# Kernel optimization log

Hardware: AMD Instinct MI355X
Metric: run time of the kernel (lower is better)

The kernel has to match this reference:

```python
import jax, jax.numpy as jnp
import numpy as np

B = 32            # graphs in batch
NPG = 2048        # nodes per graph (equal-size graphs -> static topk sizes)
N = B * NPG
DEG = 8
E = N * DEG
IN = 64
H1 = 2 * IN       # 128
H2 = 2 * H1       # 256
K1 = NPG // 2     # SAGPooling ratio=0.5
K2 = K1 // 2
EPS = 1e-5


def _lin(k, fi, fo):
    s = 1.0 / np.sqrt(fi)
    return jax.random.uniform(k, (fi, fo), jnp.float32, -s, s)


def setup_inputs() -> dict:
    key = jax.random.key(0)
    ks = jax.random.split(key, 24)
    x = jax.random.normal(ks[0], (N, IN), jnp.float32)
    # edges strictly within each graph
    eg = jnp.repeat(jnp.arange(B, dtype=jnp.int32), NPG * DEG)
    src = eg * NPG + jax.random.randint(ks[1], (E,), 0, NPG, jnp.int32)
    tgt = eg * NPG + jax.random.randint(ks[2], (E,), 0, NPG, jnp.int32)
    edge_index = jnp.stack([src, tgt])
    batch = jnp.repeat(jnp.arange(B, dtype=jnp.int32), NPG)
    return {
        "x": x, "edge_index": edge_index, "batch": batch,
        # SAGEConv1: lin_l (neighbors, with bias) + lin_r (root, no bias)
        "W1l": _lin(ks[3], IN, H1), "b1l": jnp.zeros((H1,), jnp.float32),
        "W1r": _lin(ks[4], IN, H1),
        "bn1_g": jnp.ones((H1,), jnp.float32), "bn1_b": jnp.zeros((H1,), jnp.float32),
        # SAGPooling1 scorer = GraphConv(H1, 1): lin_rel (sum-agg, bias) + lin_root
        "p1_Wrel": _lin(ks[5], H1, 1), "p1_brel": jnp.zeros((1,), jnp.float32),
        "p1_Wroot": _lin(ks[6], H1, 1),
        "W2l": _lin(ks[7], H1, H2), "b2l": jnp.zeros((H2,), jnp.float32),
        "W2r": _lin(ks[8], H1, H2),
        "bn2_g": jnp.ones((H2,), jnp.float32), "bn2_b": jnp.zeros((H2,), jnp.float32),
        "p2_Wrel": _lin(ks[9], H2, 1), "p2_brel": jnp.zeros((1,), jnp.float32),
        "p2_Wroot": _lin(ks[10], H2, 1),
        "Wlin": _lin(ks[11], H2, 2), "blin": jnp.zeros((2,), jnp.float32),
    }


def sage_conv(x, src, tgt, emask, Wl, bl, Wr, n):
    # PyG SAGEConv: mean-aggregate x_j over valid incoming edges, then lin_l(agg)+lin_r(x)
    msg = x[src] * emask[:, None]
    s = jax.ops.segment_sum(msg, tgt, num_segments=n)
    cnt = jax.ops.segment_sum(emask, tgt, num_segments=n)
    mean = s / jnp.maximum(cnt, 1.0)[:, None]
    return mean @ Wl + bl + x @ Wr


def graph_conv_score(x, src, tgt, emask, Wrel, brel, Wroot, n):
    # PyG GraphConv (sum aggregation), out_channels=1
    s = jax.ops.segment_sum(x[src] * emask[:, None], tgt, num_segments=n)
    return (s @ Wrel + brel + x @ Wroot)[:, 0]


def batch_norm(x, g, b):
    m = x.mean(0)
    v = jnp.mean((x - m) ** 2, 0)  # biased var, as BatchNorm1d training
    return (x - m) * jax.lax.rsqrt(v + EPS) * g + b


def sag_pool(x, src, tgt, emask, score, npg, k):
    # per-graph top-k by score; x_kept scaled by tanh(score); edges re-filtered via mask
    vals, idx = jax.lax.top_k(score.reshape(B, npg), k)          # [B,k]
    perm = (jnp.arange(B, dtype=jnp.int32)[:, None] * npg + idx.astype(jnp.int32)).reshape(-1)
    xnew = x[perm] * jnp.tanh(vals.reshape(-1))[:, None]
    mapping = jnp.full((x.shape[0],), -1, jnp.int32).at[perm].set(
        jnp.arange(B * k, dtype=jnp.int32))
    ns, nt = mapping[src], mapping[tgt]
    valid = emask * ((ns >= 0) & (nt >= 0)).astype(emask.dtype)
    return xnew, jnp.maximum(ns, 0), jnp.maximum(nt, 0), valid


def reference(x, edge_index, batch, W1l, b1l, W1r, bn1_g, bn1_b,
              p1_Wrel, p1_brel, p1_Wroot, W2l, b2l, W2r, bn2_g, bn2_b,
              p2_Wrel, p2_brel, p2_Wroot, Wlin, blin):
    src, tgt = edge_index[0], edge_index[1]
    emask = jnp.ones((src.shape[0],), x.dtype)

    h = sage_conv(x, src, tgt, emask, W1l, b1l, W1r, N)
    h = jax.nn.relu(batch_norm(h, bn1_g, bn1_b))
    s1 = graph_conv_score(h, src, tgt, emask, p1_Wrel, p1_brel, p1_Wroot, N)
    h, src, tgt, emask = sag_pool(h, src, tgt, emask, s1, NPG, K1)

    n1 = B * K1
    h = sage_conv(h, src, tgt, emask, W2l, b2l, W2r, n1)
    h = jax.nn.relu(batch_norm(h, bn2_g, bn2_b))
    s2 = graph_conv_score(h, src, tgt, emask, p2_Wrel, p2_brel, p2_Wroot, n1)
    h, src, tgt, emask = sag_pool(h, src, tgt, emask, s2, K1, K2)

    batch2 = jnp.repeat(jnp.arange(B, dtype=jnp.int32), K2)
    pooled = jax.ops.segment_sum(h, batch2, num_segments=B) / jnp.asarray(K2, h.dtype)
    out = jax.nn.relu(pooled) @ Wlin + blin
    return jax.nn.softmax(out, axis=1)
```

## Files before the change

kernel.cpp:

```cpp
#include <hip/hip_runtime.h>
#include <math.h>

#define Bg   32
#define NPGc 2048
#define Nn   (Bg*NPGc)
#define DEGc 8
#define Ee   (Nn*DEGc)
#define INc  64
#define H1c  128
#define H2c  256
#define K1c  1024
#define K2c  512
#define N1c  (Bg*K1c)
#define N2c  (Bg*K2c)
#define SLAB 64

typedef __attribute__((ext_vector_type(8))) short short8;
typedef __attribute__((ext_vector_type(4))) float f32x4;

__device__ __forceinline__ ushort f2bf(float f) {
    uint u = __float_as_uint(f);
    uint r = (u + 0x7fffu + ((u >> 16) & 1u)) >> 16;
    return (ushort)r;
}
__device__ __forceinline__ float bf2f(ushort v) { return __uint_as_float((uint)v << 16); }
__device__ __forceinline__ float bfhi(uint v) { return __uint_as_float(v & 0xffff0000u); }
__device__ __forceinline__ float bflo(uint v) { return __uint_as_float(v << 16); }
__device__ __forceinline__ uint fkey(float f) {
    uint u = __float_as_uint(f);
    return u ^ ((uint)((int)u >> 31) | 0x80000000u);
}

__global__ void init_kernel(int4* __restrict__ wc1, int4* __restrict__ wc2,
                            int4* __restrict__ dstats) {
    int id = blockIdx.x * blockDim.x + threadIdx.x;
    int4 z = {0, 0, 0, 0};
    if (id < 16384) { wc1[id] = z; return; }
    id -= 16384;
    if (id < 8192)  { wc2[id] = z; return; }
    id -= 8192;
    if (id < 384)   { dstats[id] = z; }
}

__global__ void prep2_kernel(const float* __restrict__ x,
                             const int* __restrict__ src, const int* __restrict__ tgt,
                             const float* __restrict__ W1l, const float* __restrict__ W1r,
                             const float* __restrict__ W2l, const float* __restrict__ W2r,
                             ushort* __restrict__ T1l, ushort* __restrict__ T1r,
                             ushort* __restrict__ T2l, ushort* __restrict__ T2r,
                             ushort* __restrict__ xb, int* __restrict__ wc1,
                             int* __restrict__ col1) {
    int id = blockIdx.x * blockDim.x + threadIdx.x;
    if (id < Ee) {
        int t = tgt[id];
        int p = atomicAdd(&wc1[t], 1);
        col1[t * SLAB + p] = src[id];
        return;
    }
    id -= Ee;
    if (id < 8192) {
        int c = id / 64, k = id % 64;
        T1l[id] = f2bf(W1l[k * 128 + c]);
        T1r[id] = f2bf(W1r[k * 128 + c]);
        return;
    }
    id -= 8192;
    if (id < 32768) {
        int c = id / 128, k = id % 128;
        T2l[id] = f2bf(W2l[k * 256 + c]);
        T2r[id] = f2bf(W2r[k * 256 + c]);
        return;
    }
    id -= 32768;
    if (id < Nn * 16) {
        float4 v = ((const float4*)x)[id];
        ushort4 o; o.x = f2bf(v.x); o.y = f2bf(v.y); o.z = f2bf(v.z); o.w = f2bf(v.w);
        ((ushort4*)xb)[id] = o;
    }
}
#define PREP2_TOTAL (Ee + 8192 + 32768 + Nn*16)

__device__ __forceinline__ void acc8(float* a, uint4 v) {
    a[0] += bflo(v.x); a[1] += bfhi(v.x);
    a[2] += bflo(v.y); a[3] += bfhi(v.y);
    a[4] += bflo(v.z); a[5] += bfhi(v.z);
    a[6] += bflo(v.w); a[7] += bfhi(v.w);
}
__device__ __forceinline__ uint4 pack8(const float* a, float inv) {
    uint4 o;
    o.x = (uint)f2bf(a[0] * inv) | ((uint)f2bf(a[1] * inv) << 16);
    o.y = (uint)f2bf(a[2] * inv) | ((uint)f2bf(a[3] * inv) << 16);
    o.z = (uint)f2bf(a[4] * inv) | ((uint)f2bf(a[5] * inv) << 16);
    o.w = (uint)f2bf(a[6] * inv) | ((uint)f2bf(a[7] * inv) << 16);
    return o;
}

__global__ void agg1_kernel(const ushort* __restrict__ xb, const int* __restrict__ deg,
                            const int* __restrict__ col, ushort* __restrict__ out) {
    int b = blockIdx.x;
    int w = ((b & 7) << 8) + (b >> 3);
    int gid = w * 256 + threadIdx.x;
    int node = gid >> 3, ln = gid & 7;
    int bg = node * SLAB, dg = deg[node];
    int4 c0 = *(const int4*)&col[bg];
    int4 c1 = *(const int4*)&col[bg + 4];
    int idx[8] = {c0.x, c0.y, c0.z, c0.w, c1.x, c1.y, c1.z, c1.w};
    float a[8] = {0.f, 0.f, 0.f, 0.f, 0.f, 0.f, 0.f, 0.f};
#pragma unroll
    for (int j = 0; j < 8; j++)
        if (j < dg) acc8(a, *(const uint4*)&xb[((size_t)idx[j] << 6) + ln * 8]);
    for (int i = bg + 8; i < bg + dg; i++)
        acc8(a, *(const uint4*)&xb[((size_t)col[i] << 6) + ln * 8]);
    int c = dg < 1 ? 1 : dg;
    *(uint4*)&out[((size_t)node << 6) + ln * 8] = pack8(a, 1.f / (float)c);
}

__global__ void agg2_kernel(const ushort* __restrict__ xb, const int* __restrict__ deg,
                            const int* __restrict__ col, ushort* __restrict__ out) {
    int b = blockIdx.x;
    int w = ((b & 7) << 8) + (b >> 3);
    int gid = w * 256 + threadIdx.x;
    int node = gid >> 4, ln = gid & 15;
    int bg = node * SLAB, dg = deg[node];
    int4 c0 = *(const int4*)&col[bg];
    int4 c1 = *(const int4*)&col[bg + 4];
    int idx[8] = {c0.x, c0.y, c0.z, c0.w, c1.x, c1.y, c1.z, c1.w};
    float a[8] = {0.f, 0.f, 0.f, 0.f, 0.f, 0.f, 0.f, 0.f};
#pragma unroll
    for (int j = 0; j < 8; j++)
        if (j < dg) acc8(a, *(const uint4*)&xb[((size_t)idx[j] << 7) + ln * 8]);
    for (int i = bg + 8; i < bg + dg; i++)
        acc8(a, *(const uint4*)&xb[((size_t)col[i] << 7) + ln * 8]);
    int c = dg < 1 ? 1 : dg;
    *(uint4*)&out[((size_t)node << 7) + ln * 8] = pack8(a, 1.f / (float)c);
}

template<int K, int COUT, int MT>
__global__ __launch_bounds__(256) void gemm_mfma_kernel(
        const ushort* __restrict__ Aagg, const ushort* __restrict__ Ax,
        const ushort* __restrict__ Wtl, const ushort* __restrict__ Wtr,
        const float* __restrict__ bias, ushort* __restrict__ out,
        double* __restrict__ dsum, double* __restrict__ dsq) {
    __shared__ ushort As[2][128][72];
    __shared__ ushort Bs[2][64][72];
    __shared__ float bsumS[2][64], bsqS[2][64];
    int bid = blockIdx.x;
    int m0 = (bid % MT) * 128;
    int c0 = (bid / MT) * 64;
    int lane = threadIdx.x & 63;
    int wid = threadIdx.x >> 6;
    int wr = (wid & 1) * 64, wc = (wid >> 1) * 32;
    int l16 = lane & 15, quad = lane >> 4;

    f32x4 acc[4][2];
#pragma unroll
    for (int a = 0; a < 4; a++)
#pragma unroll
        for (int b = 0; b < 2; b++) acc[a][b] = (f32x4){0.f, 0.f, 0.f, 0.f};

    for (int kk0 = 0; kk0 < K; kk0 += 64) {
        for (int idx = threadIdx.x; idx < 1024; idx += 256) {
            int r = idx >> 3, ck = (idx & 7) * 8;
            *(uint4*)&As[0][r][ck] = *(const uint4*)&Aagg[(size_t)(m0 + r) * K + kk0 + ck];
            *(uint4*)&As[1][r][ck] = *(const uint4*)&Ax[(size_t)(m0 + r) * K + kk0 + ck];
        }
        for (int idx = threadIdx.x; idx < 512; idx += 256) {
            int r = idx >> 3, ck = (idx & 7) * 8;
            *(uint4*)&Bs[0][r][ck] = *(const uint4*)&Wtl[(size_t)(c0 + r) * K + kk0 + ck];
            *(uint4*)&Bs[1][r][ck] = *(const uint4*)&Wtr[(size_t)(c0 + r) * K + kk0 + ck];
        }
        __syncthreads();
#pragma unroll
        for (int kk = 0; kk < 64; kk += 32) {
            short8 a[2][4], b[2][2];
#pragma unroll
            for (int s = 0; s < 2; s++)
#pragma unroll
                for (int mt = 0; mt < 4; mt++)
                    a[s][mt] = *(const short8*)&As[s][wr + mt * 16 + l16][kk + quad * 8];
#pragma unroll
            for (int s = 0; s < 2; s++)
#pragma unroll
                for (int nt = 0; nt < 2; nt++)
                    b[s][nt] = *(const short8*)&Bs[s][wc + nt * 16 + l16][kk + quad * 8];
#pragma unroll
            for (int mt = 0; mt < 4; mt++)
#pragma unroll
                for (int nt = 0; nt < 2; nt++) {
                    acc[mt][nt] = __builtin_amdgcn_mfma_f32_16x16x32_bf16(
                        a[0][mt], b[0][nt], acc[mt][nt], 0, 0, 0);
                    acc[mt][nt] = __builtin_amdgcn_mfma_f32_16x16x32_bf16(
                        a[1][mt], b[1][nt], acc[mt][nt], 0, 0, 0);
                }
        }
        __syncthreads();
    }
    float s[2] = {0.f, 0.f}, sq[2] = {0.f, 0.f};
#pragma unroll
    for (int nt = 0; nt < 2; nt++) {
        int col = c0 + wc + nt * 16 + l16;
        float bv = bias[col];
#pragma unroll
        for (int mt = 0; mt < 4; mt++)
#pragma unroll
            for (int r = 0; r < 4; r++) {
                int row = m0 + wr + mt * 16 + quad * 4 + r;
                float ov = acc[mt][nt][r] + bv;
                out[(size_t)row * COUT + col] = f2bf(ov);
                s[nt] += ov; sq[nt] += ov * ov;
            }
    }
#pragma unroll
    for (int nt = 0; nt < 2; nt++) {
        float ss = s[nt], qq = sq[nt];
        ss += __shfl_down(ss, 16); qq += __shfl_down(qq, 16);
        ss += __shfl_down(ss, 32); qq += __shfl_down(qq, 32);
        if (quad == 0) {
            bsumS[wid & 1][wc + nt * 16 + l16] = ss;
            bsqS[wid & 1][wc + nt * 16 + l16] = qq;
        }
    }
    __syncthreads();
    if (threadIdx.x < 64) {
        int c = threadIdx.x;
        atomicAdd(&dsum[c0 + c], (double)(bsumS[0][c] + bsumS[1][c]));
        atomicAdd(&dsq[c0 + c], (double)(bsqS[0][c] + bsqS[1][c]));
    }
}

template<int C>
__global__ __launch_bounds__(256) void score_kernel(const ushort* __restrict__ h,
                                                    const double* __restrict__ dsum,
                                                    const double* __restrict__ dsq,
                                                    const float* __restrict__ g,
                                                    const float* __restrict__ b,
                                                    const float* __restrict__ wrel,
                                                    const float* __restrict__ wroot,
                                                    float* __restrict__ r,
                                                    float* __restrict__ root, int n) {
    __shared__ float sc[C], sh[C], wrl[C], wrt[C];
    if ((int)threadIdx.x < C) {
        int c = threadIdx.x;
        double m = dsum[c] / (double)n;
        double var = dsq[c] / (double)n - m * m;
        float s = g[c] * (float)(1.0 / sqrt(var + 1e-5));
        sc[c] = s; sh[c] = b[c] - (float)m * s;
        wrl[c] = wrel[c]; wrt[c] = wroot[c];
    }
    __syncthreads();
    int gid = blockIdx.x * 256 + threadIdx.x;
    int node = gid >> 3, ln = gid & 7;
    float rr = 0.f, rt = 0.f;
#pragma unroll
    for (int p = 0; p < C / 64; p++) {
        int cb = p * 64 + ln * 8;
        uint4 v = *(const uint4*)&h[(size_t)node * C + cb];
        float vv[8] = {bflo(v.x), bfhi(v.x), bflo(v.y), bfhi(v.y),
                       bflo(v.z), bfhi(v.z), bflo(v.w), bfhi(v.w)};
#pragma unroll
        for (int q = 0; q < 8; q++) {
            int cc = cb + q;
            float val = fmaxf(vv[q] * sc[cc] + sh[cc], 0.f);
            rr += val * wrl[cc];
            rt += val * wrt[cc];
        }
    }
#pragma unroll
    for (int off = 4; off; off >>= 1) {
        rr += __shfl_down(rr, off);
        rt += __shfl_down(rt, off);
    }
    if (ln == 0) { r[node] = rr; root[node] = rt; }
}

__global__ void __launch_bounds__(1024) sel1_kernel(const float* __restrict__ r,
                                                    const float* __restrict__ root,
                                                    const int* __restrict__ deg,
                                                    const int* __restrict__ col,
                                                    const float* __restrict__ brel,
                                                    int* __restrict__ perm,
                                                    float* __restrict__ tval,
                                                    int* __restrict__ map) {
    __shared__ float svals[2048];
    __shared__ uint hist[257];
    __shared__ uint wsum[16];
    __shared__ uint s_b, s_rem;
    int g = blockIdx.x;
    int tid = threadIdx.x;
    int lane = tid & 63, wid = tid >> 6;
    int base = g * NPGc;
    float bv = brel[0];
#pragma unroll
    for (int j = 0; j < 2; j++) {
        int i = tid + (j << 10);
        int node = base + i;
        float acc = bv + root[node];
        int e0 = node * SLAB, dg = deg[node];
        int4 c0 = *(const int4*)&col[e0];
        int4 c1 = *(const int4*)&col[e0 + 4];
        int idx[8] = {c0.x, c0.y, c0.z, c0.w, c1.x, c1.y, c1.z, c1.w};
#pragma unroll
        for (int q = 0; q < 8; q++)
            if (q < dg) acc += r[idx[q]];
        for (int e = e0 + 8; e < e0 + dg; e++) acc += r[col[e]];
        svals[i] = acc;
    }
    if (tid < 257) hist[tid] = 0;
    __syncthreads();

    uint prefix = 0, himask = 0, rem = (uint)K1c;
    for (int shift = 24; shift >= 0; shift -= 8) {
#pragma unroll
        for (int j = 0; j < 2; j++) {
            uint kk = fkey(svals[tid + (j << 10)]);
            if ((kk & himask) == prefix) atomicAdd(&hist[(kk >> shift) & 255], 1);
        }
        __syncthreads();
        if (tid < 64) {
            int L = tid;
            uint h0 = hist[4 * L], h1 = hist[4 * L + 1], h2 = hist[4 * L + 2],
                 h3 = hist[4 * L + 3];
            uint s3 = h3, s2 = h2 + s3, s1 = h1 + s2, s0 = h0 + s1;
            uint v = s0;
            for (int off = 1; off < 64; off <<= 1) {
                uint u = __shfl_down(v, off);
                if (L + off < 64) v += u;
            }
            uint above = v - s0;
            hist[4 * L] = s0 + above;
            hist[4 * L + 1] = s1 + above;
            hist[4 * L + 2] = s2 + above;
            hist[4 * L + 3] = s3 + above;
        }
        __syncthreads();
        if (tid < 256) {
            uint sb = hist[tid], sb1 = hist[tid + 1];
            if (sb >= rem && sb1 < rem) { s_b = (uint)tid; s_rem = rem - sb1; }
        }
        __syncthreads();
        prefix |= (s_b << shift);
        rem = s_rem;
        himask |= (0xFFu << shift);
        if (tid < 256) hist[tid] = 0;
        __syncthreads();
    }
    uint thr = prefix;
    uint tieM = rem;
    uint gcnt = 0, ecnt = 0, gflags = 0, eflags = 0;
#pragma unroll
    for (int j = 0; j < 2; j++) {
        uint kk = fkey(svals[tid + (j << 10)]);
        if (kk > thr) { gflags |= 1u << j; gcnt++; }
        else if (kk == thr) { eflags |= 1u << j; ecnt++; }
    }
    uint key = (gcnt << 16) | ecnt;
    uint v = key;
    for (int off = 1; off < 64; off <<= 1) {
        uint u = __shfl_up(v, off);
        if (lane >= off) v += u;
    }
    if (lane == 63) wsum[wid] = v;
    __syncthreads();
    if (tid < 16) {
        uint w0 = wsum[tid], w = w0;
        for (int off = 1; off < 16; off <<= 1) {
            uint u = __shfl_up(w, off);
            if ((int)tid >= off) w += u;
        }
        wsum[tid] = w - w0;
    }
    __syncthreads();
    uint excl = (v - key) + wsum[wid];
    uint gbase = excl >> 16, ebase = excl & 0xFFFFu;
#pragma unroll
    for (int j = 0; j < 2; j++) {
        bool gt = (gflags >> j) & 1u;
        bool eq = (eflags >> j) & 1u;
        int i = tid + (j << 10);
        int o = -1;
        if (gt || (eq && ebase < tieM)) {
            uint pos = gbase + min(ebase, tieM);
            o = g * K1c + (int)pos;
            perm[o] = base + i;
            tval[o] = tanhf(svals[i]);
        }
        map[base + i] = o;
        gbase += gt ? 1u : 0u;
        ebase += eq ? 1u : 0u;
    }
}

__global__ void __launch_bounds__(256) mid_kernel(
        const int* __restrict__ src, const int* __restrict__ tgt,
        const int* __restrict__ map1, int* __restrict__ wc2, int* __restrict__ col2,
        const ushort* __restrict__ h1, const int* __restrict__ perm1,
        const float* __restrict__ tv1, const double* __restrict__ dsum,
        const double* __restrict__ dsq, const float* __restrict__ g,
        const float* __restrict__ b, ushort* __restrict__ h1pb) {
    __shared__ float sc[128], sh[128];
    int blk = blockIdx.x;
    if (blk < 2048) {
        int e = blk * 256 + threadIdx.x;
        int nt = map1[tgt[e]];
        int ns = map1[src[e]];
        if (nt < 0 || ns < 0) return;
        int p = atomicAdd(&wc2[nt], 1);
        col2[nt * SLAB + p] = ns;
        return;
    }
    if (threadIdx.x < 128) {
        int c = threadIdx.x;
        double m = dsum[c] / (double)Nn;
        double var = dsq[c] / (double)Nn - m * m;
        float s = g[c] * (float)(1.0 / sqrt(var + 1e-5));
        sc[c] = s; sh[c] = b[c] - (float)m * s;
    }
    __syncthreads();
    int t = (blk - 2048) * 256 + threadIdx.x;
    int m = t >> 7, c = t & 127;
    float v = fmaxf(bf2f(h1[((size_t)perm1[m] << 7) + c]) * sc[c] + sh[c], 0.f);
    h1pb[t] = f2bf(v * tv1[m]);
}

__global__ void __launch_bounds__(1024) sel2pool_kernel(
        const float* __restrict__ r, const float* __restrict__ root,
        const int* __restrict__ deg, const int* __restrict__ col,
        const float* __restrict__ brel, const ushort* __restrict__ h2,
        const double* __restrict__ dsum, const double* __restrict__ dsq,
        const float* __restrict__ g_, const float* __restrict__ b_,
        const float* __restrict__ Wlin, const float* __restrict__ blin,
        float* __restrict__ out) {
    __shared__ float svals[1024];
    __shared__ uint hist[257];
    __shared__ uint wsum[16];
    __shared__ uint s_b, s_rem;
    __shared__ int permL[512];
    __shared__ float tvL[512];
    __shared__ float sc[256], sh[256];
    __shared__ float part[4][256];
    int g = blockIdx.x;
    int tid = threadIdx.x;
    int lane = tid & 63, wid = tid >> 6;
    if (tid < 256) {
        int c = tid;
        double m = dsum[c] / (double)N1c;
        double var = dsq[c] / (double)N1c - m * m;
        float s = g_[c] * (float)(1.0 / sqrt(var + 1e-5));
        sc[c] = s; sh[c] = b_[c] - (float)m * s;
    }
    {
        int node = g * K1c + tid;
        float acc = brel[0] + root[node];
        int e0 = node * SLAB, dg = deg[node];
        int4 c0 = *(const int4*)&col[e0];
        int4 c1 = *(const int4*)&col[e0 + 4];
        int idx[8] = {c0.x, c0.y, c0.z, c0.w, c1.x, c1.y, c1.z, c1.w};
#pragma unroll
        for (int q = 0; q < 8; q++)
            if (q < dg) acc += r[idx[q]];
        for (int e = e0 + 8; e < e0 + dg; e++) acc += r[col[e]];
        svals[tid] = acc;
    }
    if (tid < 257) hist[tid] = 0;
    __syncthreads();

    uint prefix = 0, himask = 0, rem = (uint)K2c;
    for (int shift = 24; shift >= 0; shift -= 8) {
        {
            uint kk = fkey(svals[tid]);
            if ((kk & himask) == prefix) atomicAdd(&hist[(kk >> shift) & 255], 1);
        }
        __syncthreads();
        if (tid < 64) {
            int L = tid;
            uint h0 = hist[4 * L], h1 = hist[4 * L + 1], h2v = hist[4 * L + 2],
                 h3 = hist[4 * L + 3];
            uint s3 = h3, s2 = h2v + s3, s1 = h1 + s2, s0 = h0 + s1;
            uint v = s0;
            for (int off = 1; off < 64; off <<= 1) {
                uint u = __shfl_down(v, off);
                if (L + off < 64) v += u;
            }
            uint above = v - s0;
            hist[4 * L] = s0 + above;
            hist[4 * L + 1] = s1 + above;
            hist[4 * L + 2] = s2 + above;
            hist[4 * L + 3] = s3 + above;
        }
        __syncthreads();
        if (tid < 256) {
            uint sb = hist[tid], sb1 = hist[tid + 1];
            if (sb >= rem && sb1 < rem) { s_b = (uint)tid; s_rem = rem - sb1; }
        }
        __syncthreads();
        prefix |= (s_b << shift);
        rem = s_rem;
        himask |= (0xFFu << shift);
        if (tid < 256) hist[tid] = 0;
        __syncthreads();
    }
    uint thr = prefix;
    uint tieM = rem;

    uint kk = fkey(svals[tid]);
    bool gt = kk > thr, eq = kk == thr;
    uint key = (gt ? 0x10000u : 0u) | (eq ? 1u : 0u);
    uint v = key;
    for (int off = 1; off < 64; off <<= 1) {
        uint u = __shfl_up(v, off);
        if (lane >= off) v += u;
    }
    if (lane == 63) wsum[wid] = v;
    __syncthreads();
    if (tid < 16) {
        uint w0 = wsum[tid], w = w0;
        for (int off = 1; off < 16; off <<= 1) {
            uint u = __shfl_up(w, off);
            if ((int)tid >= off) w += u;
        }
        wsum[tid] = w - w0;
    }
    __syncthreads();
    uint excl = (v - key) + wsum[wid];
    uint gbase = excl >> 16, ebase = excl & 0xFFFFu;
    if (gt || (eq && ebase < tieM)) {
        uint pos = gbase + min(ebase, tieM);
        permL[pos] = g * K1c + tid;
        tvL[pos] = tanhf(svals[tid]);
    }
    __syncthreads();

    int c = tid & 255, grp = tid >> 8;
    float s = 0.f;
#pragma unroll 4
    for (int j = grp * 128; j < grp * 128 + 128; j++) {
        int row = permL[j];
        float hv = fmaxf(bf2f(h2[((size_t)row << 8) + c]) * sc[c] + sh[c], 0.f);
        s += hv * tvL[j];
    }
    part[grp][c] = s;
    __syncthreads();
    if (tid < 256) {
        float pc = part[0][tid] + part[1][tid] + part[2][tid] + part[3][tid];
        float sv = fmaxf(pc * (1.f / (float)K2c), 0.f);
        part[0][tid] = sv * Wlin[tid * 2 + 0];
        part[1][tid] = sv * Wlin[tid * 2 + 1];
    }
    __syncthreads();
    for (int off = 128; off; off >>= 1) {
        if (tid < off) { part[0][tid] += part[0][tid + off]; part[1][tid] += part[1][tid + off]; }
        __syncthreads();
    }
    if (tid == 0) {
        float o0 = part[0][0] + blin[0], o1 = part[1][0] + blin[1];
        float m = fmaxf(o0, o1);
        float e0 = expf(o0 - m), e1 = expf(o1 - m);
        float inv = 1.f / (e0 + e1);
        out[g * 2 + 0] = e0 * inv;
        out[g * 2 + 1] = e1 * inv;
    }
}

extern "C" void kernel_launch(void* const* d_in, const int* in_sizes, int n_in,
                              void* d_out, int out_size, void* d_ws, size_t ws_size,
                              hipStream_t stream) {
    const float* x      = (const float*)d_in[0];
    const int*   ei     = (const int*)d_in[1];
    const int*   src    = ei;
    const int*   tgt    = ei + Ee;
    const float* W1l    = (const float*)d_in[3];
    const float* b1l    = (const float*)d_in[4];
    const float* W1r    = (const float*)d_in[5];
    const float* bn1g   = (const float*)d_in[6];
    const float* bn1b   = (const float*)d_in[7];
    const float* p1Wrel = (const float*)d_in[8];
    const float* p1brel = (const float*)d_in[9];
    const float* p1Wroot= (const float*)d_in[10];
    const float* W2l    = (const float*)d_in[11];
    const float* b2l    = (const float*)d_in[12];
    const float* W2r    = (const float*)d_in[13];
    const float* bn2g   = (const float*)d_in[14];
    const float* bn2b   = (const float*)d_in[15];
    const float* p2Wrel = (const float*)d_in[16];
    const float* p2brel = (const float*)d_in[17];
    const float* p2Wroot= (const float*)d_in[18];
    const float* Wlin   = (const float*)d_in[19];
    const float* blin   = (const float*)d_in[20];
    float* out = (float*)d_out;
    char* ws = (char*)d_ws;

    size_t o = 0;
    auto A = [&](size_t b) { size_t r = o; o += (b + 255) & ~(size_t)255; return r; };
    size_t oBIG1 = A((size_t)Nn * H1c * 2);
    size_t oBIG2 = A((size_t)Nn * INc * 4);
    size_t oPB   = A((size_t)N1c * H1c * 4);
    size_t oCol1 = A((size_t)Nn * SLAB * 4);
    size_t oCol2 = A((size_t)N1c * SLAB * 4);
    size_t oWc1  = A((size_t)Nn * 4);
    size_t oR1   = A((size_t)Nn * 4);
    size_t oRoot1= A((size_t)Nn * 4);
    size_t oMap1 = A((size_t)Nn * 4);
    size_t oPerm1= A((size_t)N1c * 4);
    size_t oTv1  = A((size_t)N1c * 4);
    size_t oWc2  = A((size_t)N1c * 4);
    size_t oR2   = A((size_t)N1c * 4);
    size_t oRoot2= A((size_t)N1c * 4);
    size_t oDst  = A(768 * 8);
    size_t oWt1l = A(8192 * 2);
    size_t oWt1r = A(8192 * 2);
    size_t oWt2l = A(32768 * 2);
    size_t oWt2r = A(32768 * 2);
    (void)ws_size; (void)in_sizes; (void)n_in; (void)out_size;

    ushort* h1   = (ushort*)(ws + oBIG1);
    ushort* h2   = (ushort*)(ws + oBIG1);
    ushort* xb   = (ushort*)(ws + oBIG2);
    ushort* aggb1= (ushort*)(ws + oBIG2 + (size_t)Nn * 64 * 2);
    ushort* h1pb = (ushort*)(ws + oPB);
    ushort* aggb2= (ushort*)(ws + oPB + (size_t)N1c * 128 * 2);
    int* col1    = (int*)(ws + oCol1);
    int* col2    = (int*)(ws + oCol2);
    int* wc1     = (int*)(ws + oWc1);
    float* r1    = (float*)(ws + oR1);
    float* root1 = (float*)(ws + oRoot1);
    int* map1    = (int*)(ws + oMap1);
    int* perm1   = (int*)(ws + oPerm1);
    float* tv1   = (float*)(ws + oTv1);
    int* wc2     = (int*)(ws + oWc2);
    float* r2    = (float*)(ws + oR2);
    float* root2 = (float*)(ws + oRoot2);
    double* dsum1= (double*)(ws + oDst);
    double* dsq1 = dsum1 + 128;
    double* dsum2= dsum1 + 256;
    double* dsq2 = dsum1 + 512;
    ushort* T1l  = (ushort*)(ws + oWt1l);
    ushort* T1r  = (ushort*)(ws + oWt1r);
    ushort* T2l  = (ushort*)(ws + oWt2l);
    ushort* T2r  = (ushort*)(ws + oWt2r);

    init_kernel<<<98, 256, 0, stream>>>((int4*)wc1, (int4*)wc2, (int4*)dsum1);

    prep2_kernel<<<PREP2_TOTAL / 256, 256, 0, stream>>>(
        x, src, tgt, W1l, W1r, W2l, W2r, T1l, T1r, T2l, T2r, xb, wc1, col1);

    agg1_kernel<<<2048, 256, 0, stream>>>(xb, wc1, col1, aggb1);
    gemm_mfma_kernel<INc, H1c, 512><<<1024, 256, 0, stream>>>(aggb1, xb, T1l, T1r, b1l,
                                                              h1, dsum1, dsq1);

    score_kernel<H1c><<<Nn / 32, 256, 0, stream>>>(h1, dsum1, dsq1, bn1g, bn1b, p1Wrel,
                                                   p1Wroot, r1, root1, Nn);
    sel1_kernel<<<Bg, 1024, 0, stream>>>(r1, root1, wc1, col1, p1brel, perm1, tv1, map1);
    mid_kernel<<<2048 + (N1c * H1c) / 256, 256, 0, stream>>>(
        src, tgt, map1, wc2, col2, h1, perm1, tv1, dsum1, dsq1, bn1g, bn1b, h1pb);

    agg2_kernel<<<2048, 256, 0, stream>>>(h1pb, wc2, col2, aggb2);
    gemm_mfma_kernel<H1c, H2c, 256><<<1024, 256, 0, stream>>>(aggb2, h1pb, T2l, T2r, b2l,
                                                              h2, dsum2, dsq2);

    score_kernel<H2c><<<N1c / 32, 256, 0, stream>>>(h2, dsum2, dsq2, bn2g, bn2b, p2Wrel,
                                                    p2Wroot, r2, root2, N1c);
    sel2pool_kernel<<<Bg, 1024, 0, stream>>>(r2, root2, wc2, col2, p2brel, h2, dsum2,
                                             dsq2, bn2g, bn2b, Wlin, blin, out);
}
```

Measured before the change: 259.7 us.

## Fuse neighbor aggregation into GEMMs and scoring into top-k selection kernels

Folds the mean-aggregation gather straight into the MFMA GEMM kernels. Each block now covers the full output width and builds the aggregated A tile in shared memory, so the aggregated bf16 buffers no longer go through global memory. It also merges the BN+ReLU+score computation into the per-graph selection kernels, keeping per-node scores in LDS so r/root arrays are gone. This cuts four launches and intermediate traffic. In exchange, selection runs on only 32 blocks that must now read all of h1/h2, the GEMM grids are smaller, and gather latency sits inside the GEMM loop.

New measurement: 345.1 us. 1.33x slower.

```diff
diff --git a/kernel.cpp b/kernel.cpp
--- a/kernel.cpp
+++ b/kernel.cpp
@@ -95,118 +95,93 @@
     return o;
 }
 
-__global__ void agg1_kernel(const ushort* __restrict__ xb, const int* __restrict__ deg,
-                            const int* __restrict__ col, ushort* __restrict__ out) {
+__global__ __launch_bounds__(512) void gemm1f_kernel(
+        const ushort* __restrict__ xb, const int* __restrict__ deg,
+        const int* __restrict__ col, const ushort* __restrict__ Wtl,
+        const ushort* __restrict__ Wtr, const float* __restrict__ bias,
+        ushort* __restrict__ out, double* __restrict__ dsum,
+        double* __restrict__ dsq) {
+    __shared__ ushort As[2][128][36];
+    __shared__ ushort Bs[2][128][36];
+    __shared__ float bsumS[2][128], bsqS[2][128];
     int b = blockIdx.x;
-    int w = ((b & 7) << 8) + (b >> 3);
-    int gid = w * 256 + threadIdx.x;
-    int node = gid >> 3, ln = gid & 7;
-    int bg = node * SLAB, dg = deg[node];
-    int4 c0 = *(const int4*)&col[bg];
-    int4 c1 = *(const int4*)&col[bg + 4];
-    int idx[8] = {c0.x, c0.y, c0.z, c0.w, c1.x, c1.y, c1.z, c1.w};
-    float a[8] = {0.f, 0.f, 0.f, 0.f, 0.f, 0.f, 0.f, 0.f};
-#pragma unroll
-    for (int j = 0; j < 8; j++)
-        if (j < dg) acc8(a, *(const uint4*)&xb[((size_t)idx[j] << 6) + ln * 8]);
-    for (int i = bg + 8; i < bg + dg; i++)
-        acc8(a, *(const uint4*)&xb[((size_t)col[i] << 6) + ln * 8]);
-    int c = dg < 1 ? 1 : dg;
-    *(uint4*)&out[((size_t)node << 6) + ln * 8] = pack8(a, 1.f / (float)c);
-}
-
-__global__ void agg2_kernel(const ushort* __restrict__ xb, const int* __restrict__ deg,
-                            const int* __restrict__ col, ushort* __restrict__ out) {
-    int b = blockIdx.x;
-    int w = ((b & 7) << 8) + (b >> 3);
-    int gid = w * 256 + threadIdx.x;
-    int node = gid >> 4, ln = gid & 15;
-    int bg = node * SLAB, dg = deg[node];
-    int4 c0 = *(const int4*)&col[bg];
-    int4 c1 = *(const int4*)&col[bg + 4];
-    int idx[8] = {c0.x, c0.y, c0.z, c0.w, c1.x, c1.y, c1.z, c1.w};
-    float a[8] = {0.f, 0.f, 0.f, 0.f, 0.f, 0.f, 0.f, 0.f};
-#pragma unroll
-    for (int j = 0; j < 8; j++)
-        if (j < dg) acc8(a, *(const uint4*)&xb[((size_t)idx[j] << 7) + ln * 8]);
-    for (int i = bg + 8; i < bg + dg; i++)
-        acc8(a, *(const uint4*)&xb[((size_t)col[i] << 7) + ln * 8]);
-    int c = dg < 1 ? 1 : dg;
-    *(uint4*)&out[((size_t)node << 7) + ln * 8] = pack8(a, 1.f / (float)c);
-}
-
-template<int K, int COUT, int MT>
-__global__ __launch_bounds__(256) void gemm_mfma_kernel(
-        const ushort* __restrict__ Aagg, const ushort* __restrict__ Ax,
-        const ushort* __restrict__ Wtl, const ushort* __restrict__ Wtr,
-        const float* __restrict__ bias, ushort* __restrict__ out,
-        double* __restrict__ dsum, double* __restrict__ dsq) {
-    __shared__ ushort As[2][128][72];
-    __shared__ ushort Bs[2][64][72];
-    __shared__ float bsumS[2][64], bsqS[2][64];
-    int bid = blockIdx.x;
-    int m0 = (bid % MT) * 128;
-    int c0 = (bid / MT) * 64;
+    int bs = ((b & 7) << 6) + (b >> 3);
+    int m0 = bs << 7;
     int lane = threadIdx.x & 63;
     int wid = threadIdx.x >> 6;
-    int wr = (wid & 1) * 64, wc = (wid >> 1) * 32;
+    int wr = (wid & 1) << 6, wc = (wid >> 1) << 5;
     int l16 = lane & 15, quad = lane >> 4;
 
     f32x4 acc[4][2];
 #pragma unroll
     for (int a = 0; a < 4; a++)
 #pragma unroll
-        for (int b = 0; b < 2; b++) acc[a][b] = (f32x4){0.f, 0.f, 0.f, 0.f};
-
-    for (int kk0 = 0; kk0 < K; kk0 += 64) {
-        for (int idx = threadIdx.x; idx < 1024; idx += 256) {
-            int r = idx >> 3, ck = (idx & 7) * 8;
-            *(uint4*)&As[0][r][ck] = *(const uint4*)&Aagg[(size_t)(m0 + r) * K + kk0 + ck];
-            *(uint4*)&As[1][r][ck] = *(const uint4*)&Ax[(size_t)(m0 + r) * K + kk0 + ck];
-        }
-        for (int idx = threadIdx.x; idx < 512; idx += 256) {
-            int r = idx >> 3, ck = (idx & 7) * 8;
-            *(uint4*)&Bs[0][r][ck] = *(const uint4*)&Wtl[(size_t)(c0 + r) * K + kk0 + ck];
-            *(uint4*)&Bs[1][r][ck] = *(const uint4*)&Wtr[(size_t)(c0 + r) * K + kk0 + ck];
-        }
-        __syncthreads();
-#pragma unroll
-        for (int kk = 0; kk < 64; kk += 32) {
-            short8 a[2][4], b[2][2];
-#pragma unroll
-            for (int s = 0; s < 2; s++)
-#pragma unroll
-                for (int mt = 0; mt < 4; mt++)
-                    a[s][mt] = *(const short8*)&As[s][wr + mt * 16 + l16][kk + quad * 8];
-#pragma unroll
-            for (int s = 0; s < 2; s++)
-#pragma unroll
-                for (int nt = 0; nt < 2; nt++)
-                    b[s][nt] = *(const short8*)&Bs[s][wc + nt * 16 + l16][kk + quad * 8];
+        for (int c = 0; c < 2; c++) acc[a][c] = (f32x4){0.f, 0.f, 0.f, 0.f};
+
+    for (int kk0 = 0; kk0 < INc; kk0 += 32) {
+        {
+            int idx = threadIdx.x;
+            int r = idx >> 2, ck = (idx & 3) * 8;
+            *(uint4*)&Bs[0][r][ck] = *(const uint4*)&Wtl[(size_t)r * INc + kk0 + ck];
+            *(uint4*)&Bs[1][r][ck] = *(const uint4*)&Wtr[(size_t)r * INc + kk0 + ck];
+        }
+        {
+            int idx = threadIdx.x;
+            int r = idx >> 2, ck = (idx & 3) * 8;
+            *(uint4*)&As[1][r][ck] = *(const uint4*)&xb[((size_t)(m0 + r) << 6) + kk0 + ck];
+        }
+        {
+            int idx = threadIdx.x;
+            int r = idx >> 2, ck = (idx & 3) * 8;
+            int node = m0 + r;
+            int bg = node * SLAB, dg = deg[node];
+            int4 c0 = *(const int4*)&col[bg];
+            int4 c1 = *(const int4*)&col[bg + 4];
+            int nb[8] = {c0.x, c0.y, c0.z, c0.w, c1.x, c1.y, c1.z, c1.w};
+            float a[8] = {0.f, 0.f, 0.f, 0.f, 0.f, 0.f, 0.f, 0.f};
+#pragma unroll
+            for (int j = 0; j < 8; j++)
+                if (j < dg) acc8(a, *(const uint4*)&xb[((size_t)nb[j] << 6) + kk0 + ck]);
+            for (int i = bg + 8; i < bg + dg; i++)
+                acc8(a, *(const uint4*)&xb[((size_t)col[i] << 6) + kk0 + ck]);
+            int cdg = dg < 1 ? 1 : dg;
+            *(uint4*)&As[0][r][ck] = pack8(a, 1.f / (float)cdg);
+        }
+        __syncthreads();
+        short8 a[2][4], bfr[2][2];
+#pragma unroll
+        for (int s = 0; s < 2; s++)
 #pragma unroll
             for (int mt = 0; mt < 4; mt++)
-#pragma unroll
-                for (int nt = 0; nt < 2; nt++) {
-                    acc[mt][nt] = __builtin_amdgcn_mfma_f32_16x16x32_bf16(
-                        a[0][mt], b[0][nt], acc[mt][nt], 0, 0, 0);
-                    acc[mt][nt] = __builtin_amdgcn_mfma_f32_16x16x32_bf16(
-                        a[1][mt], b[1][nt], acc[mt][nt], 0, 0, 0);
-                }
-        }
+                a[s][mt] = *(const short8*)&As[s][wr + mt * 16 + l16][quad * 8];
+#pragma unroll
+        for (int s = 0; s < 2; s++)
+#pragma unroll
+            for (int nt = 0; nt < 2; nt++)
+                bfr[s][nt] = *(const short8*)&Bs[s][wc + nt * 16 + l16][quad * 8];
+#pragma unroll
+        for (int mt = 0; mt < 4; mt++)
+#pragma unroll
+            for (int nt = 0; nt < 2; nt++) {
+                acc[mt][nt] = __builtin_amdgcn_mfma_f32_16x16x32_bf16(
+                    a[0][mt], bfr[0][nt], acc[mt][nt], 0, 0, 0);
+                acc[mt][nt] = __builtin_amdgcn_mfma_f32_16x16x32_bf16(
+                    a[1][mt], bfr[1][nt], acc[mt][nt], 0, 0, 0);
+            }
         __syncthreads();
     }
     float s[2] = {0.f, 0.f}, sq[2] = {0.f, 0.f};
 #pragma unroll
     for (int nt = 0; nt < 2; nt++) {
-        int col = c0 + wc + nt * 16 + l16;
-        float bv = bias[col];
+        int colx = wc + nt * 16 + l16;
+        float bv = bias[colx];
 #pragma unroll
         for (int mt = 0; mt < 4; mt++)
 #pragma unroll
-            for (int r = 0; r < 4; r++) {
-                int row = m0 + wr + mt * 16 + quad * 4 + r;
-                float ov = acc[mt][nt][r] + bv;
-                out[(size_t)row * COUT + col] = f2bf(ov);
+            for (int rr = 0; rr < 4; rr++) {
+                int row = m0 + wr + mt * 16 + quad * 4 + rr;
+                float ov = acc[mt][nt][rr] + bv;
+                out[(size_t)row * H1c + colx] = f2bf(ov);
                 s[nt] += ov; sq[nt] += ov * ov;
             }
     }
@@ -221,91 +196,78 @@
         }
     }
     __syncthreads();
-    if (threadIdx.x < 64) {
+    if (threadIdx.x < 128) {
         int c = threadIdx.x;
-        atomicAdd(&dsum[c0 + c], (double)(bsumS[0][c] + bsumS[1][c]));
-        atomicAdd(&dsq[c0 + c], (double)(bsqS[0][c] + bsqS[1][c]));
-    }
-}
-
-template<int C>
-__global__ __launch_bounds__(256) void score_kernel(const ushort* __restrict__ h,
-                                                    const double* __restrict__ dsum,
-                                                    const double* __restrict__ dsq,
-                                                    const float* __restrict__ g,
-                                                    const float* __restrict__ b,
-                                                    const float* __restrict__ wrel,
-                                                    const float* __restrict__ wroot,
-                                                    float* __restrict__ r,
-                                                    float* __restrict__ root, int n) {
-    __shared__ float sc[C], sh[C], wrl[C], wrt[C];
-    if ((int)threadIdx.x < C) {
-        int c = threadIdx.x;
-        double m = dsum[c] / (double)n;
-        double var = dsq[c] / (double)n - m * m;
-        float s = g[c] * (float)(1.0 / sqrt(var + 1e-5));
-        sc[c] = s; sh[c] = b[c] - (float)m * s;
-        wrl[c] = wrel[c]; wrt[c] = wroot[c];
-    }
-    __syncthreads();
-    int gid = blockIdx.x * 256 + threadIdx.x;
-    int node = gid >> 3, ln = gid & 7;
-    float rr = 0.f, rt = 0.f;
-#pragma unroll
-    for (int p = 0; p < C / 64; p++) {
-        int cb = p * 64 + ln * 8;
-        uint4 v = *(const uint4*)&h[(size_t)node * C + cb];
-        float vv[8] = {bflo(v.x), bfhi(v.x), bflo(v.y), bfhi(v.y),
-                       bflo(v.z), bfhi(v.z), bflo(v.w), bfhi(v.w)};
-#pragma unroll
-        for (int q = 0; q < 8; q++) {
-            int cc = cb + q;
-            float val = fmaxf(vv[q] * sc[cc] + sh[cc], 0.f);
-            rr += val * wrl[cc];
-            rt += val * wrt[cc];
-        }
-    }
-#pragma unroll
-    for (int off = 4; off; off >>= 1) {
-        rr += __shfl_down(rr, off);
-        rt += __shfl_down(rt, off);
-    }
-    if (ln == 0) { r[node] = rr; root[node] = rt; }
-}
-
-__global__ void __launch_bounds__(1024) sel1_kernel(const float* __restrict__ r,
-                                                    const float* __restrict__ root,
-                                                    const int* __restrict__ deg,
-                                                    const int* __restrict__ col,
-                                                    const float* __restrict__ brel,
-                                                    int* __restrict__ perm,
-                                                    float* __restrict__ tval,
-                                                    int* __restrict__ map) {
+        atomicAdd(&dsum[c], (double)(bsumS[0][c] + bsumS[1][c]));
+        atomicAdd(&dsq[c], (double)(bsqS[0][c] + bsqS[1][c]));
+    }
+}
+
+__global__ void __launch_bounds__(1024) sel1f_kernel(
+        const ushort* __restrict__ h1, const double* __restrict__ dsum,
+        const double* __restrict__ dsq, const float* __restrict__ bng,
+        const float* __restrict__ bnb, const float* __restrict__ wrel,
+        const float* __restrict__ wroot, const float* __restrict__ brel,
+        const int* __restrict__ deg, const int* __restrict__ col,
+        int* __restrict__ perm, float* __restrict__ tval, int* __restrict__ map) {
+    __shared__ float sc[128], sh[128], wrl[128], wrt[128];
+    __shared__ float rL[2048];
     __shared__ float svals[2048];
     __shared__ uint hist[257];
     __shared__ uint wsum[16];
     __shared__ uint s_b, s_rem;
-    int g = blockIdx.x;
+    int g = ((blockIdx.x & 7) << 2) + (blockIdx.x >> 3);
     int tid = threadIdx.x;
     int lane = tid & 63, wid = tid >> 6;
     int base = g * NPGc;
+    if (tid < 128) {
+        int c = tid;
+        double m = dsum[c] / (double)Nn;
+        double var = dsq[c] / (double)Nn - m * m;
+        float s = bng[c] * (float)(1.0 / sqrt(var + 1e-5));
+        sc[c] = s; sh[c] = bnb[c] - (float)m * s;
+        wrl[c] = wrel[c]; wrt[c] = wroot[c];
+    }
+    if (tid < 257) hist[tid] = 0;
+    __syncthreads();
+    float rootv[2];
+#pragma unroll
+    for (int j = 0; j < 2; j++) {
+        int i = tid + (j << 10);
+        const ushort* hp = &h1[(size_t)(base + i) << 7];
+        float rr = 0.f, rt = 0.f;
+#pragma unroll
+        for (int cb = 0; cb < 128; cb += 8) {
+            uint4 v = *(const uint4*)&hp[cb];
+            float vv[8] = {bflo(v.x), bfhi(v.x), bflo(v.y), bfhi(v.y),
+                           bflo(v.z), bfhi(v.z), bflo(v.w), bfhi(v.w)};
+#pragma unroll
+            for (int q = 0; q < 8; q++) {
+                int cc = cb + q;
+                float val = fmaxf(vv[q] * sc[cc] + sh[cc], 0.f);
+                rr += val * wrl[cc];
+                rt += val * wrt[cc];
+            }
+        }
+        rL[i] = rr; rootv[j] = rt;
+    }
+    __syncthreads();
     float bv = brel[0];
 #pragma unroll
     for (int j = 0; j < 2; j++) {
         int i = tid + (j << 10);
         int node = base + i;
-        float acc = bv + root[node];
+        float acc = bv + rootv[j];
         int e0 = node * SLAB, dg = deg[node];
         int4 c0 = *(const int4*)&col[e0];
         int4 c1 = *(const int4*)&col[e0 + 4];
-        int idx[8] = {c0.x, c0.y, c0.z, c0.w, c1.x, c1.y, c1.z, c1.w};
+        int nb[8] = {c0.x, c0.y, c0.z, c0.w, c1.x, c1.y, c1.z, c1.w};
 #pragma unroll
         for (int q = 0; q < 8; q++)
-            if (q < dg) acc += r[idx[q]];
-        for (int e = e0 + 8; e < e0 + dg; e++) acc += r[col[e]];
+            if (q < dg) acc += rL[nb[q] - base];
+        for (int e = e0 + 8; e < e0 + dg; e++) acc += rL[col[e] - base];
         svals[i] = acc;
     }
-    if (tid < 257) hist[tid] = 0;
     __syncthreads();
 
     uint prefix = 0, himask = 0, rem = (uint)K1c;
@@ -318,9 +280,9 @@
         __syncthreads();
         if (tid < 64) {
             int L = tid;
-            uint h0 = hist[4 * L], h1 = hist[4 * L + 1], h2 = hist[4 * L + 2],
+            uint h0 = hist[4 * L], h1v = hist[4 * L + 1], h2v = hist[4 * L + 2],
                  h3 = hist[4 * L + 3];
-            uint s3 = h3, s2 = h2 + s3, s1 = h1 + s2, s0 = h0 + s1;
+            uint s3 = h3, s2 = h2v + s3, s1 = h1v + s2, s0 = h0 + s1;
             uint v = s0;
             for (int off = 1; off < 64; off <<= 1) {
                 uint u = __shfl_down(v, off);
@@ -422,46 +384,178 @@
     h1pb[t] = f2bf(v * tv1[m]);
 }
 
-__global__ void __launch_bounds__(1024) sel2pool_kernel(
-        const float* __restrict__ r, const float* __restrict__ root,
+__global__ __launch_bounds__(512) void gemm2f_kernel(
+        const ushort* __restrict__ h1pb, const int* __restrict__ deg,
+        const int* __restrict__ col, const ushort* __restrict__ Wtl,
+        const ushort* __restrict__ Wtr, const float* __restrict__ bias,
+        ushort* __restrict__ out, double* __restrict__ dsum,
+        double* __restrict__ dsq) {
+    __shared__ ushort As[2][128][36];
+    __shared__ ushort Bs[2][256][36];
+    __shared__ float bsumS[2][256], bsqS[2][256];
+    int b = blockIdx.x;
+    int bs = ((b & 7) << 5) + (b >> 3);
+    int m0 = bs << 7;
+    int lane = threadIdx.x & 63;
+    int wid = threadIdx.x >> 6;
+    int wr = (wid & 1) << 6, wc = (wid >> 1) << 6;
+    int l16 = lane & 15, quad = lane >> 4;
+
+    f32x4 acc[4][4];
+#pragma unroll
+    for (int a = 0; a < 4; a++)
+#pragma unroll
+        for (int c = 0; c < 4; c++) acc[a][c] = (f32x4){0.f, 0.f, 0.f, 0.f};
+
+    for (int kk0 = 0; kk0 < H1c; kk0 += 32) {
+        for (int idx = threadIdx.x; idx < 1024; idx += 512) {
+            int r = idx >> 2, ck = (idx & 3) * 8;
+            *(uint4*)&Bs[0][r][ck] = *(const uint4*)&Wtl[(size_t)r * H1c + kk0 + ck];
+            *(uint4*)&Bs[1][r][ck] = *(const uint4*)&Wtr[(size_t)r * H1c + kk0 + ck];
+        }
+        {
+            int idx = threadIdx.x;
+            int r = idx >> 2, ck = (idx & 3) * 8;
+            *(uint4*)&As[1][r][ck] =
+                *(const uint4*)&h1pb[((size_t)(m0 + r) << 7) + kk0 + ck];
+        }
+        {
+            int idx = threadIdx.x;
+            int r = idx >> 2, ck = (idx & 3) * 8;
+            int node = m0 + r;
+            int bg = node * SLAB, dg = deg[node];
+            int4 c0 = *(const int4*)&col[bg];
+            int4 c1 = *(const int4*)&col[bg + 4];
+            int nb[8] = {c0.x, c0.y, c0.z, c0.w, c1.x, c1.y, c1.z, c1.w};
+            float a[8] = {0.f, 0.f, 0.f, 0.f, 0.f, 0.f, 0.f, 0.f};
+#pragma unroll
+            for (int j = 0; j < 8; j++)
+                if (j < dg) acc8(a, *(const uint4*)&h1pb[((size_t)nb[j] << 7) + kk0 + ck]);
+            for (int i = bg + 8; i < bg + dg; i++)
+                acc8(a, *(const uint4*)&h1pb[((size_t)col[i] << 7) + kk0 + ck]);
+            int cdg = dg < 1 ? 1 : dg;
+            *(uint4*)&As[0][r][ck] = pack8(a, 1.f / (float)cdg);
+        }
+        __syncthreads();
+        short8 a[2][4], bfr[2][4];
+#pragma unroll
+        for (int s = 0; s < 2; s++)
+#pragma unroll
+            for (int mt = 0; mt < 4; mt++)
+                a[s][mt] = *(const short8*)&As[s][wr + mt * 16 + l16][quad * 8];
+#pragma unroll
+        for (int s = 0; s < 2; s++)
+#pragma unroll
+            for (int nt = 0; nt < 4; nt++)
+                bfr[s][nt] = *(const short8*)&Bs[s][wc + nt * 16 + l16][quad * 8];
+#pragma unroll
+        for (int mt = 0; mt < 4; mt++)
+#pragma unroll
+            for (int nt = 0; nt < 4; nt++) {
+                acc[mt][nt] = __builtin_amdgcn_mfma_f32_16x16x32_bf16(
+                    a[0][mt], bfr[0][nt], acc[mt][nt], 0, 0, 0);
+                acc[mt][nt] = __builtin_amdgcn_mfma_f32_16x16x32_bf16(
+                    a[1][mt], bfr[1][nt], acc[mt][nt], 0, 0, 0);
+            }
+        __syncthreads();
+    }
+    float s[4] = {0.f, 0.f, 0.f, 0.f}, sq[4] = {0.f, 0.f, 0.f, 0.f};
+#pragma unroll
+    for (int nt = 0; nt < 4; nt++) {
+        int colx = wc + nt * 16 + l16;
+        float bv = bias[colx];
+#pragma unroll
+        for (int mt = 0; mt < 4; mt++)
+#pragma unroll
+            for (int rr = 0; rr < 4; rr++) {
+                int row = m0 + wr + mt * 16 + quad * 4 + rr;
+                float ov = acc[mt][nt][rr] + bv;
+                out[(size_t)row * H2c + colx] = f2bf(ov);
+                s[nt] += ov; sq[nt] += ov * ov;
+            }
+    }
+#pragma unroll
+    for (int nt = 0; nt < 4; nt++) {
+        float ss = s[nt], qq = sq[nt];
+        ss += __shfl_down(ss, 16); qq += __shfl_down(qq, 16);
+        ss += __shfl_down(ss, 32); qq += __shfl_down(qq, 32);
+        if (quad == 0) {
+            bsumS[wid & 1][wc + nt * 16 + l16] = ss;
+            bsqS[wid & 1][wc + nt * 16 + l16] = qq;
+        }
+    }
+    __syncthreads();
+    if (threadIdx.x < 256) {
+        int c = threadIdx.x;
+        atomicAdd(&dsum[c], (double)(bsumS[0][c] + bsumS[1][c]));
+        atomicAdd(&dsq[c], (double)(bsqS[0][c] + bsqS[1][c]));
+    }
+}
+
+__global__ void __launch_bounds__(1024) sel2poolf_kernel(
+        const ushort* __restrict__ h2, const double* __restrict__ dsum,
+        const double* __restrict__ dsq, const float* __restrict__ bng,
+        const float* __restrict__ bnb, const float* __restrict__ wrel,
+        const float* __restrict__ wroot, const float* __restrict__ brel,
         const int* __restrict__ deg, const int* __restrict__ col,
-        const float* __restrict__ brel, const ushort* __restrict__ h2,
-        const double* __restrict__ dsum, const double* __restrict__ dsq,
-        const float* __restrict__ g_, const float* __restrict__ b_,
         const float* __restrict__ Wlin, const float* __restrict__ blin,
         float* __restrict__ out) {
+    __shared__ float sc[256], sh[256], wrl[256], wrt[256];
+    __shared__ float rL[1024];
     __shared__ float svals[1024];
     __shared__ uint hist[257];
     __shared__ uint wsum[16];
     __shared__ uint s_b, s_rem;
     __shared__ int permL[512];
     __shared__ float tvL[512];
-    __shared__ float sc[256], sh[256];
     __shared__ float part[4][256];
-    int g = blockIdx.x;
+    int g = ((blockIdx.x & 7) << 2) + (blockIdx.x >> 3);
     int tid = threadIdx.x;
     int lane = tid & 63, wid = tid >> 6;
+    int base = g * K1c;
     if (tid < 256) {
         int c = tid;
         double m = dsum[c] / (double)N1c;
         double var = dsq[c] / (double)N1c - m * m;
-        float s = g_[c] * (float)(1.0 / sqrt(var + 1e-5));
-        sc[c] = s; sh[c] = b_[c] - (float)m * s;
-    }
+        float s = bng[c] * (float)(1.0 / sqrt(var + 1e-5));
+        sc[c] = s; sh[c] = bnb[c] - (float)m * s;
+        wrl[c] = wrel[c]; wrt[c] = wroot[c];
+    }
+    if (tid < 257) hist[tid] = 0;
+    __syncthreads();
+    float rootv;
     {
-        int node = g * K1c + tid;
-        float acc = brel[0] + root[node];
+        const ushort* hp = &h2[(size_t)(base + tid) << 8];
+        float rr = 0.f, rt = 0.f;
+#pragma unroll 4
+        for (int cb = 0; cb < 256; cb += 8) {
+            uint4 v = *(const uint4*)&hp[cb];
+            float vv[8] = {bflo(v.x), bfhi(v.x), bflo(v.y), bfhi(v.y),
+                           bflo(v.z), bfhi(v.z), bflo(v.w), bfhi(v.w)};
+#pragma unroll
+            for (int q = 0; q < 8; q++) {
+                int cc = cb + q;
+                float val = fmaxf(vv[q] * sc[cc] + sh[cc], 0.f);
+                rr += val * wrl[cc];
+                rt += val * wrt[cc];
+            }
+        }
+        rL[tid] = rr; rootv = rt;
+    }
+    __syncthreads();
+    {
+        int node = base + tid;
+        float acc = brel[0] + rootv;
         int e0 = node * SLAB, dg = deg[node];
         int4 c0 = *(const int4*)&col[e0];
         int4 c1 = *(const int4*)&col[e0 + 4];
-        int idx[8] = {c0.x, c0.y, c0.z, c0.w, c1.x, c1.y, c1.z, c1.w};
+        int nb[8] = {c0.x, c0.y, c0.z, c0.w, c1.x, c1.y, c1.z, c1.w};
 #pragma unroll
         for (int q = 0; q < 8; q++)
-            if (q < dg) acc += r[idx[q]];
-        for (int e = e0 + 8; e < e0 + dg; e++) acc += r[col[e]];
+            if (q < dg) acc += rL[nb[q] - base];
+        for (int e = e0 + 8; e < e0 + dg; e++) acc += rL[col[e] - base];
         svals[tid] = acc;
     }
-    if (tid < 257) hist[tid] = 0;
     __syncthreads();
 
     uint prefix = 0, himask = 0, rem = (uint)K2c;
@@ -473,9 +567,9 @@
         __syncthreads();
         if (tid < 64) {
             int L = tid;
-            uint h0 = hist[4 * L], h1 = hist[4 * L + 1], h2v = hist[4 * L + 2],
+            uint h0 = hist[4 * L], h1v = hist[4 * L + 1], h2v = hist[4 * L + 2],
                  h3 = hist[4 * L + 3];
-            uint s3 = h3, s2 = h2v + s3, s1 = h1 + s2, s0 = h0 + s1;
+            uint s3 = h3, s2 = h2v + s3, s1 = h1v + s2, s0 = h0 + s1;
             uint v = s0;
             for (int off = 1; off < 64; off <<= 1) {
                 uint u = __shfl_down(v, off);
@@ -525,7 +619,7 @@
     uint gbase = excl >> 16, ebase = excl & 0xFFFFu;
     if (gt || (eq && ebase < tieM)) {
         uint pos = gbase + min(ebase, tieM);
-        permL[pos] = g * K1c + tid;
+        permL[pos] = base + tid;
         tvL[pos] = tanhf(svals[tid]);
     }
     __syncthreads();
@@ -592,19 +686,15 @@
     size_t o = 0;
     auto A = [&](size_t b) { size_t r = o; o += (b + 255) & ~(size_t)255; return r; };
     size_t oBIG1 = A((size_t)Nn * H1c * 2);
-    size_t oBIG2 = A((size_t)Nn * INc * 4);
-    size_t oPB   = A((size_t)N1c * H1c * 4);
+    size_t oXB   = A((size_t)Nn * INc * 2);
+    size_t oPB   = A((size_t)N1c * H1c * 2);
     size_t oCol1 = A((size_t)Nn * SLAB * 4);
     size_t oCol2 = A((size_t)N1c * SLAB * 4);
     size_t oWc1  = A((size_t)Nn * 4);
-    size_t oR1   = A((size_t)Nn * 4);
-    size_t oRoot1= A((size_t)Nn * 4);
     size_t oMap1 = A((size_t)Nn * 4);
     size_t oPerm1= A((size_t)N1c * 4);
     size_t oTv1  = A((size_t)N1c * 4);
     size_t oWc2  = A((size_t)N1c * 4);
-    size_t oR2   = A((size_t)N1c * 4);
-    size_t oRoot2= A((size_t)N1c * 4);
     size_t oDst  = A(768 * 8);
     size_t oWt1l = A(8192 * 2);
     size_t oWt1r = A(8192 * 2);
@@ -614,21 +704,15 @@
 
     ushort* h1   = (ushort*)(ws + oBIG1);
     ushort* h2   = (ushort*)(ws + oBIG1);
-    ushort* xb   = (ushort*)(ws + oBIG2);
-    ushort* aggb1= (ushort*)(ws + oBIG2 + (size_t)Nn * 64 * 2);
+    ushort* xb   = (ushort*)(ws + oXB);
     ushort* h1pb = (ushort*)(ws + oPB);
-    ushort* aggb2= (ushort*)(ws + oPB + (size_t)N1c * 128 * 2);
     int* col1    = (int*)(ws + oCol1);
     int* col2    = (int*)(ws + oCol2);
     int* wc1     = (int*)(ws + oWc1);
-    float* r1    = (float*)(ws + oR1);
-    float* root1 = (float*)(ws + oRoot1);
     int* map1    = (int*)(ws + oMap1);
     int* perm1   = (int*)(ws + oPerm1);
     float* tv1   = (float*)(ws + oTv1);
     int* wc2     = (int*)(ws + oWc2);
-    float* r2    = (float*)(ws + oR2);
-    float* root2 = (float*)(ws + oRoot2);
     double* dsum1= (double*)(ws + oDst);
     double* dsq1 = dsum1 + 128;
     double* dsum2= dsum1 + 256;
@@ -643,22 +727,19 @@
     prep2_kernel<<<PREP2_TOTAL / 256, 256, 0, stream>>>(
         x, src, tgt, W1l, W1r, W2l, W2r, T1l, T1r, T2l, T2r, xb, wc1, col1);
 
-    agg1_kernel<<<2048, 256, 0, stream>>>(xb, wc1, col1, aggb1);
-    gemm_mfma_kernel<INc, H1c, 512><<<1024, 256, 0, stream>>>(aggb1, xb, T1l, T1r, b1l,
-                                                              h1, dsum1, dsq1);
-
-    score_kernel<H1c><<<Nn / 32, 256, 0, stream>>>(h1, dsum1, dsq1, bn1g, bn1b, p1Wrel,
-                                                   p1Wroot, r1, root1, Nn);
-    sel1_kernel<<<Bg, 1024, 0, stream>>>(r1, root1, wc1, col1, p1brel, perm1, tv1, map1);
+    gemm1f_kernel<<<512, 512, 0, stream>>>(xb, wc1, col1, T1l, T1r, b1l, h1,
+                                           dsum1, dsq1);
+
+    sel1f_kernel<<<Bg, 1024, 0, stream>>>(h1, dsum1, dsq1, bn1g, bn1b, p1Wrel, p1Wroot,
+                                          p1brel, wc1, col1, perm1, tv1, map1);
+
     mid_kernel<<<2048 + (N1c * H1c) / 256, 256, 0, stream>>>(
         src, tgt, map1, wc2, col2, h1, perm1, tv1, dsum1, dsq1, bn1g, bn1b, h1pb);
 
-    agg2_kernel<<<2048, 256, 0, stream>>>(h1pb, wc2, col2, aggb2);
-    gemm_mfma_kernel<H1c, H2c, 256><<<1024, 256, 0, stream>>>(aggb2, h1pb, T2l, T2r, b2l,
-                                                              h2, dsum2, dsq2);
-
-    score_kernel<H2c><<<N1c / 32, 256, 0, stream>>>(h2, dsum2, dsq2, bn2g, bn2b, p2Wrel,
-                                                    p2Wroot, r2, root2, N1c);
-    sel2pool_kernel<<<Bg, 1024, 0, stream>>>(r2, root2, wc2, col2, p2brel, h2, dsum2,
-                                             dsq2, bn2g, bn2b, Wlin, blin, out);
-}
+    gemm2f_kernel<<<256, 512, 0, stream>>>(h1pb, wc2, col2, T2l, T2r, b2l, h2,
+                                           dsum2, dsq2);
+
+    sel2poolf_kernel<<<Bg, 1024, 0, stream>>>(h2, dsum2, dsq2, bn2g, bn2b, p2Wrel,
+                                              p2Wroot, p2brel, wc2, col2, Wlin, blin,
+                                              out);
+}
```
